# Performance work log

Hardware: AMD Instinct MI355X
Metric: run time of the kernel (lower is better)

## Reference

```python
import jax, jax.numpy as jnp
import numpy as np

DIM = 768
HEADS = 12
HEAD_DIM = DIM // HEADS
SCALE = HEAD_DIM ** -0.5
H_CONST = 4  # 'h' in the reaction term


def setup_inputs() -> dict:
    key = jax.random.key(0)
    ks = jax.random.split(key, 9)
    B, N = 4, 1024
    s = DIM ** -0.5
    return {
        "x": jax.random.normal(ks[0], (B, N, DIM), dtype=jnp.float32),
        "qkv_w": jax.random.normal(ks[1], (3 * DIM, DIM), dtype=jnp.float32) * s,
        "proj_l_w": jax.random.normal(ks[2], (HEADS, HEADS), dtype=jnp.float32) * HEADS ** -0.5,
        "proj_l_b": jax.random.normal(ks[3], (HEADS,), dtype=jnp.float32) * 0.02,
        "proj_w_w": jax.random.normal(ks[4], (HEADS, HEADS), dtype=jnp.float32) * HEADS ** -0.5,
        "proj_w_b": jax.random.normal(ks[5], (HEADS,), dtype=jnp.float32) * 0.02,
        "lamb": jax.random.normal(ks[6], (HEADS,), dtype=jnp.float32) * 0.1,
        "proj_out_w": jax.random.normal(ks[7], (DIM, DIM), dtype=jnp.float32) * s,
        "proj_out_b": jax.random.normal(ks[8], (DIM,), dtype=jnp.float32) * 0.02,
    }


def reference(x, qkv_w, proj_l_w, proj_l_b, proj_w_w, proj_w_b, lamb,
              proj_out_w, proj_out_b):
    B, N, C = x.shape
    # qkv: [B,N,3C] -> [B,N,3,H,hd] -> q,k,v each [B,H,N,hd]
    qkv = (x @ qkv_w.T).reshape(B, N, 3, HEADS, HEAD_DIM)
    qkv = jnp.transpose(qkv, (2, 0, 3, 1, 4))
    q, k, v = qkv[0] * SCALE, qkv[1], qkv[2]
    # raw scores [B,H,N,N]
    attn = jnp.einsum('bhnd,bhmd->bhnm', q, k)
    # pre-softmax talking-heads mix (Linear over head axis)
    attn = jnp.einsum('bhnm,gh->bgnm', attn, proj_l_w) + proj_l_b[:, None, None]
    attn = jax.nn.softmax(attn, axis=-1)
    # post-softmax talking-heads mix
    attn = jnp.einsum('bhnm,gh->bgnm', attn, proj_w_w) + proj_w_b[:, None, None]
    # GFSA reaction: (h-1)*(attn - I) @ attn + attn, scaled by per-head lamb
    eye = jnp.eye(N, dtype=attn.dtype)[None, None]
    reaction = (H_CONST - 1) * jnp.einsum('bhnk,bhkm->bhnm', attn - eye, attn) + attn
    attn = attn + lamb[None, :, None, None] * reaction
    # weighted values -> [B,N,C] -> output projection
    out = jnp.einsum('bhnm,bhmd->bhnd', attn, v)
    out = jnp.transpose(out, (0, 2, 1, 3)).reshape(B, N, C)
    return out @ proj_out_w.T + proj_out_b
```

## Files before the change

kernel.cpp:

```cpp
#include <hip/hip_runtime.h>
#include <hip/hip_bf16.h>


typedef __bf16 bf16x8 __attribute__((ext_vector_type(8)));
typedef float f32x4 __attribute__((ext_vector_type(4)));

#define DI __device__ __forceinline__

DI unsigned short f2bf(float f) {
  union { float f; unsigned u; } x; x.f = f;
  unsigned r = x.u + 0x7FFF + ((x.u >> 16) & 1);
  return (unsigned short)(r >> 16);
}
DI float bf2f(unsigned short u) {
  union { unsigned u; float f; } x; x.u = ((unsigned)u) << 16; return x.f;
}
DI float bfu_lo(unsigned u) {
  union { unsigned u; float f; } x; x.u = u << 16; return x.f;
}
DI float bfu_hi(unsigned u) {
  union { unsigned u; float f; } x; x.u = u & 0xffff0000u; return x.f;
}
DI unsigned pk_bf16(float a, float b) {
  unsigned r;
  asm("v_cvt_pk_bf16_f32 %0, %1, %2" : "=v"(r) : "v"(a), "v"(b));
  return r;
}
DI void gload16(const unsigned short* g, unsigned short* l) {
  __builtin_amdgcn_global_load_lds(
      (const __attribute__((address_space(1))) unsigned int*)g,
      (__attribute__((address_space(3))) unsigned int*)l, 16, 0, 0);
}

struct GP {
  const unsigned short* A;
  const unsigned short* B;
  int K, lda, ldb, ldc;
  long sA, sB, sC;
  unsigned short* C;
  const unsigned short* C2;
  float* outF;
  const float* bias;
  const float* lamb;
  unsigned short* q_out;
  unsigned short* k_out;
  unsigned short* vT_out;
};

template<int WM, int WN, int FM, int FN, int EPI, int STC>
__global__ __launch_bounds__(256) void gemm_bt(GP p) {
  constexpr int BM = WM * FM * 16, BN = WN * FN * 16;
  constexpr int LSZ = (BM * 64 + BN * 64) > (BM * BN) ? (BM * 64 + BN * 64)
                                                      : (BM * BN);
  __shared__ __align__(16) unsigned short ls[LSZ];
  unsigned short* lA = ls;
  unsigned short* lB = ls + BM * 64;
  const int tid = threadIdx.x, lane = tid & 63, wid = tid >> 6;
  const int wr = wid / WN, wc = wid % WN;
  const int m0 = blockIdx.y * BM, n0 = blockIdx.x * BN;
  const int bz = blockIdx.z;
  const unsigned short* Ab = p.A + (long)bz * p.sA;
  const unsigned short* Bb = p.B + (long)bz * p.sB;

  f32x4 acc[FM][FN];
#pragma unroll
  for (int i = 0; i < FM; ++i)
#pragma unroll
    for (int j = 0; j < FN; ++j) acc[i][j] = (f32x4)0.f;

  for (int k0 = 0; k0 < p.K; k0 += 64) {
    __syncthreads();
#pragma unroll
    for (int i = 0; i < BM / 32; ++i) {
      int c = tid + i * 256, r = c >> 3, kc = c & 7, kg = kc ^ (r & 7);
      gload16(Ab + (long)(m0 + r) * p.lda + k0 + kg * 8, &lA[c * 8]);
    }
#pragma unroll
    for (int i = 0; i < BN / 32; ++i) {
      int c = tid + i * 256, r = c >> 3, kc = c & 7, kg = kc ^ (r & 7);
      gload16(Bb + (long)(n0 + r) * p.ldb + k0 + kg * 8, &lB[c * 8]);
    }
    __syncthreads();
#pragma unroll
    for (int half = 0; half < 2; ++half) {
      bf16x8 af[FM], bfr[FN];
#pragma unroll
      for (int mi = 0; mi < FM; ++mi) {
        int r = wr * FM * 16 + mi * 16 + (lane & 15);
        int kc = half * 4 + (lane >> 4);
        af[mi] = *(const bf16x8*)&lA[r * 64 + ((kc ^ (r & 7)) << 3)];
      }
#pragma unroll
      for (int ni = 0; ni < FN; ++ni) {
        int r = wc * FN * 16 + ni * 16 + (lane & 15);
        int kc = half * 4 + (lane >> 4);
        bfr[ni] = *(const bf16x8*)&lB[r * 64 + ((kc ^ (r & 7)) << 3)];
      }
#pragma unroll
      for (int mi = 0; mi < FM; ++mi)
#pragma unroll
        for (int ni = 0; ni < FN; ++ni)
          acc[mi][ni] = __builtin_amdgcn_mfma_f32_16x16x32_bf16(
              af[mi], bfr[ni], acc[mi][ni], 0, 0, 0);
    }
  }

  if constexpr (STC == 1) {
    __syncthreads();
#pragma unroll
    for (int mi = 0; mi < FM; ++mi)
#pragma unroll
      for (int ni = 0; ni < FN; ++ni) {
        int row = wr * FM * 16 + mi * 16 + (lane >> 4) * 4;
        int col = wc * FN * 16 + ni * 16 + (lane & 15);
#pragma unroll
        for (int r2 = 0; r2 < 4; ++r2)
          ls[(row + r2) * BN + (col ^ ((row + r2) & 7) * 8)] =
              f2bf(acc[mi][ni][r2]);
      }
    __syncthreads();
    constexpr int CPR = BN / 8;
#pragma unroll
    for (int idx = tid; idx < BM * CPR; idx += 256) {
      int row = idx / CPR, cc = idx % CPR;
      uint4 d = *(const uint4*)&ls[row * BN + (cc ^ (row & 7)) * 8];
      *(uint4*)&p.C[(long)bz * p.sC + (long)(m0 + row) * p.ldc + n0 + cc * 8] = d;
    }
    return;
  }

#pragma unroll
  for (int mi = 0; mi < FM; ++mi)
#pragma unroll
    for (int ni = 0; ni < FN; ++ni) {
      const int rowb = m0 + wr * FM * 16 + mi * 16 + (lane >> 4) * 4;
      const int col = n0 + wc * FN * 16 + ni * 16 + (lane & 15);
      if constexpr (EPI == 1) {
        int s = col / 768, rem = col - s * 768;
        int h = rem >> 6, d = rem & 63;
        int b = rowb >> 10, n = rowb & 1023;
        long ho = (long)(b * 12 + h);
        if (s == 2) {
          uint2 pk = { pk_bf16(acc[mi][ni][0], acc[mi][ni][1]),
                       pk_bf16(acc[mi][ni][2], acc[mi][ni][3]) };
          *(uint2*)&p.vT_out[(ho * 64 + d) * 1024 + n] = pk;
        } else {
#pragma unroll
          for (int r2 = 0; r2 < 4; ++r2) {
            float v = acc[mi][ni][r2];
            if (s == 0)
              p.q_out[(ho * 1024 + n + r2) * 64 + d] = f2bf(v * 0.125f);
            else
              p.k_out[(ho * 1024 + n + r2) * 64 + d] = f2bf(v);
          }
        }
      } else if constexpr (EPI == 2) {
        float bb = p.bias[col];
#pragma unroll
        for (int r2 = 0; r2 < 4; ++r2)
          p.outF[(long)(rowb + r2) * p.ldc + col] = acc[mi][ni][r2] + bb;
      } else if constexpr (EPI == 4) {
        int b = bz / 12, h = bz - b * 12;
        float lam = p.lamb[h];
        float a1 = 1.f - 2.f * lam, c3 = 3.f * lam;
        uint2 uq = *(const uint2*)&p.C2[(long)bz * 65536 + (long)col * 1024 + rowb];
        float uv[4] = { bf2f((unsigned short)(uq.x & 0xffff)),
                        bf2f((unsigned short)(uq.x >> 16)),
                        bf2f((unsigned short)(uq.y & 0xffff)),
                        bf2f((unsigned short)(uq.y >> 16)) };
#pragma unroll
        for (int r2 = 0; r2 < 4; ++r2) {
          float val = a1 * uv[r2] + c3 * acc[mi][ni][r2];
          p.C[((long)(b * 1024 + rowb + r2)) * 768 + h * 64 + col] = f2bf(val);
        }
      }
    }
}

__global__ __launch_bounds__(256) void mix_softmax(
    unsigned short* S, const float* W1, const float* b1,
    const float* W2, const float* b2) {
  __shared__ float part[256][13];
  __shared__ float rsum[12];
  const int tid = threadIdx.x, lane = tid & 63, wid = tid >> 6;
  const int bn = blockIdx.x;
  const int b = bn >> 10, n = bn & 1023;
  unsigned short* Sb = S + ((long)(b * 12) * 1024 + n) * 1024 + tid * 4;

  float L[12][4];
#pragma unroll
  for (int g = 0; g < 12; ++g) {
    float bb = b1[g];
#pragma unroll
    for (int j = 0; j < 4; ++j) L[g][j] = bb;
  }
#pragma unroll
  for (int h = 0; h < 12; ++h) {
    uint2 u = *(const uint2*)(Sb + (long)h * 1048576);
    float f0 = bfu_lo(u.x), f1 = bfu_hi(u.x);
    float f2 = bfu_lo(u.y), f3 = bfu_hi(u.y);
#pragma unroll
    for (int g = 0; g < 12; ++g) {
      float w = W1[g * 12 + h];
      L[g][0] += w * f0; L[g][1] += w * f1;
      L[g][2] += w * f2; L[g][3] += w * f3;
    }
  }
#pragma unroll
  for (int g = 0; g < 12; ++g) {
    L[g][0] = __expf(L[g][0]); L[g][1] = __expf(L[g][1]);
    L[g][2] = __expf(L[g][2]); L[g][3] = __expf(L[g][3]);
    part[tid][g] = (L[g][0] + L[g][1]) + (L[g][2] + L[g][3]);
  }
  __syncthreads();
#pragma unroll
  for (int i = 0; i < 3; ++i) {
    int h = wid * 3 + i;
    float s = part[lane][h] + part[lane + 64][h] +
              part[lane + 128][h] + part[lane + 192][h];
#pragma unroll
    for (int o = 32; o > 0; o >>= 1) s += __shfl_xor(s, o);
    if (lane == 0) rsum[h] = 1.f / s;
  }
  __syncthreads();
#pragma unroll
  for (int g = 0; g < 12; ++g) {
    float rinv = rsum[g];
#pragma unroll
    for (int j = 0; j < 4; ++j) L[g][j] *= rinv;
  }
#pragma unroll
  for (int g = 0; g < 12; ++g) {
    float bb = b2[g];
    float o0 = bb, o1 = bb, o2 = bb, o3 = bb;
#pragma unroll
    for (int h = 0; h < 12; ++h) {
      float w = W2[g * 12 + h];
      o0 += w * L[h][0]; o1 += w * L[h][1];
      o2 += w * L[h][2]; o3 += w * L[h][3];
    }
    uint2 ov = { pk_bf16(o0, o1), pk_bf16(o2, o3) };
    *(uint2*)(Sb + (long)g * 1048576) = ov;
  }
}

__global__ __launch_bounds__(256) void cvt3(
    const float* a, const float* b, const float* c,
    unsigned short* oa, unsigned short* ob, unsigned short* oc,
    int na, int nb, int nc) {
  int i = blockIdx.x * 256 + threadIdx.x;
  const float* src;
  unsigned short* dst;
  int j = i;
  if (i < na) { src = a; dst = oa; }
  else if (i < na + nb) { src = b; dst = ob; j = i - na; }
  else if (i < na + nb + nc) { src = c; dst = oc; j = i - na - nb; }
  else return;
  float4 v = *(const float4*)(src + (long)j * 4);
  uint2 o = { pk_bf16(v.x, v.y), pk_bf16(v.z, v.w) };
  *(uint2*)(dst + (long)j * 4) = o;
}

extern "C" void kernel_launch(void* const* d_in, const int* in_sizes, int n_in,
                              void* d_out, int out_size, void* d_ws,
                              size_t ws_size, hipStream_t stream) {
  const float* x     = (const float*)d_in[0];
  const float* qkv_w = (const float*)d_in[1];
  const float* W1    = (const float*)d_in[2];
  const float* b1    = (const float*)d_in[3];
  const float* W2    = (const float*)d_in[4];
  const float* b2    = (const float*)d_in[5];
  const float* lamb  = (const float*)d_in[6];
  const float* Wout  = (const float*)d_in[7];
  const float* bout  = (const float*)d_in[8];
  float* out = (float*)d_out;

  char* ws = (char*)d_ws;
  size_t off = 0;
  auto alloc = [&](size_t bytes) {
    char* p = ws + off;
    off = (off + bytes + 255) & ~(size_t)255;
    return p;
  };
  unsigned short* Sbuf    = (unsigned short*)alloc(48ull * 1024 * 1024 * 2);
  unsigned short* x_bf    = (unsigned short*)alloc(4096ull * 768 * 2);
  unsigned short* wqkv_bf = (unsigned short*)alloc(2304ull * 768 * 2);
  unsigned short* wout_bf = (unsigned short*)alloc(768ull * 768 * 2);
  unsigned short* q_bf    = (unsigned short*)alloc(48ull * 1024 * 64 * 2);
  unsigned short* k_bf    = (unsigned short*)alloc(48ull * 1024 * 64 * 2);
  unsigned short* vT_bf   = (unsigned short*)alloc(48ull * 64 * 1024 * 2);
  unsigned short* UT      = (unsigned short*)alloc(48ull * 64 * 1024 * 2);
  unsigned short* ctx     = (unsigned short*)alloc(4096ull * 768 * 2);
  if (off > ws_size) return;

  cvt3<<<dim3(5376), 256, 0, stream>>>(x, qkv_w, Wout, x_bf, wqkv_bf, wout_bf,
                                       786432, 442368, 147456);

  {
    GP p{};
    p.A = x_bf; p.B = wqkv_bf;
    p.K = 768; p.lda = 768; p.ldb = 768;
    p.q_out = q_bf; p.k_out = k_bf; p.vT_out = vT_bf;
    gemm_bt<2, 2, 4, 4, 1, 0><<<dim3(18, 32, 1), 256, 0, stream>>>(p);
  }
  {
    GP p{};
    p.A = q_bf; p.B = k_bf;
    p.K = 64; p.lda = 64; p.ldb = 64;
    p.sA = 65536; p.sB = 65536;
    p.C = Sbuf; p.sC = 1048576; p.ldc = 1024;
    gemm_bt<2, 2, 4, 4, 0, 1><<<dim3(8, 8, 48), 256, 0, stream>>>(p);
  }
  mix_softmax<<<dim3(4096), 256, 0, stream>>>(Sbuf, W1, b1, W2, b2);
  {
    GP p{};
    p.A = vT_bf; p.B = Sbuf;
    p.K = 1024; p.lda = 1024; p.ldb = 1024;
    p.sA = 65536; p.sB = 1048576;
    p.C = UT; p.sC = 65536; p.ldc = 1024;
    gemm_bt<1, 4, 4, 1, 0, 1><<<dim3(16, 1, 48), 256, 0, stream>>>(p);
  }
  {
    GP p{};
    p.A = Sbuf; p.B = UT;
    p.K = 1024; p.lda = 1024; p.ldb = 1024;
    p.sA = 1048576; p.sB = 65536;
    p.C = ctx; p.C2 = UT; p.lamb = lamb;
    gemm_bt<4, 1, 1, 4, 4, 0><<<dim3(1, 16, 48), 256, 0, stream>>>(p);
  }
  {
    GP p{};
    p.A = ctx; p.B = wout_bf;
    p.K = 768; p.lda = 768; p.ldb = 768;
    p.outF = out; p.bias = bout; p.ldc = 768;
    gemm_bt<2, 2, 2, 2, 2, 0><<<dim3(12, 64, 1), 256, 0, stream>>>(p);
  }
}
```

Before: 198.5 us.

## Run talking-heads head mixing on MFMA with fp16 scores staged in LDS

The QK^T score GEMM now writes fp16 instead of bf16, and mix_softmax stages each row's 12 heads into LDS. It then performs both 12x12 head-mixing matmuls with 16x16x16 f16 MFMA instructions instead of scalar FMAs. The softmax row-sum reduction is restructured around the MFMA output layout. This aims to cut the VALU-heavy mixing cost, but raw scores stored in fp16 could lose range or overflow, and the kernel needs more LDS and extra synchronisation.

```diff
diff --git a/kernel.cpp b/kernel.cpp
--- a/kernel.cpp
+++ b/kernel.cpp
@@ -4,6 +4,9 @@
 
 typedef __bf16 bf16x8 __attribute__((ext_vector_type(8)));
 typedef float f32x4 __attribute__((ext_vector_type(4)));
+typedef _Float16 half4v __attribute__((ext_vector_type(4)));
+typedef _Float16 half2v __attribute__((ext_vector_type(2)));
+typedef __fp16 fp16x2 __attribute__((ext_vector_type(2)));
 
 #define DI __device__ __forceinline__
 
@@ -15,21 +18,30 @@
 DI float bf2f(unsigned short u) {
   union { unsigned u; float f; } x; x.u = ((unsigned)u) << 16; return x.f;
 }
-DI float bfu_lo(unsigned u) {
-  union { unsigned u; float f; } x; x.u = u << 16; return x.f;
-}
-DI float bfu_hi(unsigned u) {
-  union { unsigned u; float f; } x; x.u = u & 0xffff0000u; return x.f;
+DI unsigned short f2h(float f) {
+  union { _Float16 h; unsigned short u; } x;
+  x.h = (_Float16)f;
+  return x.u;
 }
 DI unsigned pk_bf16(float a, float b) {
   unsigned r;
   asm("v_cvt_pk_bf16_f32 %0, %1, %2" : "=v"(r) : "v"(a), "v"(b));
   return r;
 }
+DI half2v pkrtz(float a, float b) {
+  fp16x2 t = __builtin_amdgcn_cvt_pkrtz(a, b);
+  union { fp16x2 a; half2v b; } u;
+  u.a = t;
+  return u.b;
+}
 DI void gload16(const unsigned short* g, unsigned short* l) {
   __builtin_amdgcn_global_load_lds(
       (const __attribute__((address_space(1))) unsigned int*)g,
       (__attribute__((address_space(3))) unsigned int*)l, 16, 0, 0);
+}
+
+DI f32x4 mfma1616(half4v a, half4v b, f32x4 c) {
+  return __builtin_amdgcn_mfma_f32_16x16x16f16(a, b, c, 0, 0, 0);
 }
 
 struct GP {
@@ -105,7 +117,7 @@
     }
   }
 
-  if constexpr (STC == 1) {
+  if constexpr (STC >= 1) {
     __syncthreads();
 #pragma unroll
     for (int mi = 0; mi < FM; ++mi)
@@ -114,9 +126,11 @@
         int row = wr * FM * 16 + mi * 16 + (lane >> 4) * 4;
         int col = wc * FN * 16 + ni * 16 + (lane & 15);
 #pragma unroll
-        for (int r2 = 0; r2 < 4; ++r2)
+        for (int r2 = 0; r2 < 4; ++r2) {
+          float v = acc[mi][ni][r2];
           ls[(row + r2) * BN + (col ^ ((row + r2) & 7) * 8)] =
-              f2bf(acc[mi][ni][r2]);
+              (STC == 2) ? f2h(v) : f2bf(v);
+        }
       }
     __syncthreads();
     constexpr int CPR = BN / 8;
@@ -180,67 +194,95 @@
 __global__ __launch_bounds__(256) void mix_softmax(
     unsigned short* S, const float* W1, const float* b1,
     const float* W2, const float* b2) {
-  __shared__ float part[256][13];
-  __shared__ float rsum[12];
+  constexpr int RS = 1028;
+  __shared__ __align__(16) unsigned short sld[16 * RS];
+  __shared__ float red[4][16];
   const int tid = threadIdx.x, lane = tid & 63, wid = tid >> 6;
-  const int bn = blockIdx.x;
-  const int b = bn >> 10, n = bn & 1023;
-  unsigned short* Sb = S + ((long)(b * 12) * 1024 + n) * 1024 + tid * 4;
-
-  float L[12][4];
-#pragma unroll
-  for (int g = 0; g < 12; ++g) {
-    float bb = b1[g];
-#pragma unroll
-    for (int j = 0; j < 4; ++j) L[g][j] = bb;
-  }
-#pragma unroll
-  for (int h = 0; h < 12; ++h) {
-    uint2 u = *(const uint2*)(Sb + (long)h * 1048576);
-    float f0 = bfu_lo(u.x), f1 = bfu_hi(u.x);
-    float f2 = bfu_lo(u.y), f3 = bfu_hi(u.y);
-#pragma unroll
-    for (int g = 0; g < 12; ++g) {
-      float w = W1[g * 12 + h];
-      L[g][0] += w * f0; L[g][1] += w * f1;
-      L[g][2] += w * f2; L[g][3] += w * f3;
-    }
-  }
-#pragma unroll
-  for (int g = 0; g < 12; ++g) {
-    L[g][0] = __expf(L[g][0]); L[g][1] = __expf(L[g][1]);
-    L[g][2] = __expf(L[g][2]); L[g][3] = __expf(L[g][3]);
-    part[tid][g] = (L[g][0] + L[g][1]) + (L[g][2] + L[g][3]);
+  const int bn = blockIdx.x, b = bn >> 10, n = bn & 1023;
+  unsigned short* Sb = S + ((long)(b * 12) * 1024 + n) * 1024;
+
+#pragma unroll
+  for (int i = 0; i < 6; ++i) {
+    int idx = tid + i * 256;
+    int row = idx >> 7, ch = idx & 127;
+    uint4 d = *(const uint4*)(Sb + (long)row * 1048576 + ch * 8);
+    uint2 lo = { d.x, d.y }, hi = { d.z, d.w };
+    *(uint2*)&sld[row * RS + ch * 8] = lo;
+    *(uint2*)&sld[row * RS + ch * 8 + 4] = hi;
+  }
+  {
+    uint2 z = { 0u, 0u };
+#pragma unroll
+    for (int i = 0; i < 5; ++i) {
+      int idx = tid + i * 256;
+      if (idx < 1028) *(uint2*)&sld[12 * RS + idx * 4] = z;
+    }
+  }
+  const int gr = lane & 15, kb = (lane >> 4) * 4;
+  half4v w1f, w2f;
+  f32x4 bias1, bias2;
+#pragma unroll
+  for (int j = 0; j < 4; ++j) {
+    int k = kb + j;
+    bool v = (gr < 12) && (k < 12);
+    w1f[j] = v ? (_Float16)W1[gr * 12 + k] : (_Float16)0.f;
+    w2f[j] = v ? (_Float16)W2[gr * 12 + k] : (_Float16)0.f;
+    bias1[j] = (k < 12) ? b1[k] : 0.f;
+    bias2[j] = (k < 12) ? b2[k] : 0.f;
   }
   __syncthreads();
-#pragma unroll
-  for (int i = 0; i < 3; ++i) {
-    int h = wid * 3 + i;
-    float s = part[lane][h] + part[lane + 64][h] +
-              part[lane + 128][h] + part[lane + 192][h];
-#pragma unroll
-    for (int o = 32; o > 0; o >>= 1) s += __shfl_xor(s, o);
-    if (lane == 0) rsum[h] = 1.f / s;
+
+  const _Float16* sh = (const _Float16*)sld;
+  const int colb = wid * 256 + (lane & 15);
+  f32x4 pv[16];
+  float ssum[4] = { 0.f, 0.f, 0.f, 0.f };
+#pragma unroll
+  for (int c = 0; c < 16; ++c) {
+    int col = colb + c * 16;
+    half4v bf;
+#pragma unroll
+    for (int j = 0; j < 4; ++j) bf[j] = sh[(kb + j) * RS + col];
+    f32x4 acc = mfma1616(w1f, bf, bias1);
+#pragma unroll
+    for (int r = 0; r < 4; ++r) {
+      float e = __expf(acc[r]);
+      pv[c][r] = e;
+      ssum[r] += e;
+    }
+  }
+#pragma unroll
+  for (int r = 0; r < 4; ++r) {
+#pragma unroll
+    for (int m = 1; m < 16; m <<= 1) ssum[r] += __shfl_xor(ssum[r], m);
+  }
+  if ((lane & 15) == 0) {
+#pragma unroll
+    for (int r = 0; r < 4; ++r) red[wid][kb + r] = ssum[r];
   }
   __syncthreads();
-#pragma unroll
-  for (int g = 0; g < 12; ++g) {
-    float rinv = rsum[g];
-#pragma unroll
-    for (int j = 0; j < 4; ++j) L[g][j] *= rinv;
-  }
-#pragma unroll
-  for (int g = 0; g < 12; ++g) {
-    float bb = b2[g];
-    float o0 = bb, o1 = bb, o2 = bb, o3 = bb;
-#pragma unroll
-    for (int h = 0; h < 12; ++h) {
-      float w = W2[g * 12 + h];
-      o0 += w * L[h][0]; o1 += w * L[h][1];
-      o2 += w * L[h][2]; o3 += w * L[h][3];
-    }
-    uint2 ov = { pk_bf16(o0, o1), pk_bf16(o2, o3) };
-    *(uint2*)(Sb + (long)g * 1048576) = ov;
+  float rinv[4];
+#pragma unroll
+  for (int r = 0; r < 4; ++r)
+    rinv[r] = 1.f / (red[0][kb + r] + red[1][kb + r] +
+                     red[2][kb + r] + red[3][kb + r]);
+#pragma unroll
+  for (int c = 0; c < 16; ++c) {
+    int col = colb + c * 16;
+    union { half4v h4; half2v h2[2]; } pf;
+    pf.h2[0] = pkrtz(pv[c][0] * rinv[0], pv[c][1] * rinv[1]);
+    pf.h2[1] = pkrtz(pv[c][2] * rinv[2], pv[c][3] * rinv[3]);
+    f32x4 o = mfma1616(w2f, pf.h4, bias2);
+#pragma unroll
+    for (int r = 0; r < 4; ++r)
+      sld[(kb + r) * RS + col] = (unsigned short)(pk_bf16(o[r], o[r]) & 0xffffu);
+  }
+  __syncthreads();
+#pragma unroll
+  for (int i = 0; i < 12; ++i) {
+    int idx = tid + i * 256;
+    int row = idx >> 8, ch = idx & 255;
+    *(uint2*)(Sb + (long)row * 1048576 + ch * 4) =
+        *(const uint2*)&sld[row * RS + ch * 4];
   }
 }
 
@@ -309,7 +351,7 @@
     p.K = 64; p.lda = 64; p.ldb = 64;
     p.sA = 65536; p.sB = 65536;
     p.C = Sbuf; p.sC = 1048576; p.ldc = 1024;
-    gemm_bt<2, 2, 4, 4, 0, 1><<<dim3(8, 8, 48), 256, 0, stream>>>(p);
+    gemm_bt<2, 2, 4, 4, 0, 2><<<dim3(8, 8, 48), 256, 0, stream>>>(p);
   }
   mix_softmax<<<dim3(4096), 256, 0, stream>>>(Sbuf, W1, b1, W2, b2);
   {
```

Measured after the change: 179.6 us. 9.5% less time.
